# Kernel tuning notes

Hardware: AMD Instinct MI355X
Metric: run time of the kernel (lower is better)

The kernel has to match this reference:

```python
import jax, jax.numpy as jnp
import numpy as np
from jax import lax

MU = 0.1          # cfg MODEL.MU (FISTA step size)
LMBD = 0.1        # cfg MODEL.LAMBDA[0]
N_STEPS = 4       # cfg MODEL.NUM_LAYERS (unrolled FISTA iterations)
BN_EPS = 1e-5


def _norm_w(W):
    # DictBlock w_norm: each dictionary filter normalized to unit L2 norm.
    # torch does this under no_grad (in-place on .data), so the norm is a constant.
    n = jnp.sqrt(jnp.sum(W * W, axis=(1, 2, 3), keepdims=True))
    return W / lax.stop_gradient(n + 1e-12)


def _conv(x, W, stride, pad):
    return lax.conv_general_dilated(x, W, (stride, stride), [(pad, pad)] * 2,
                                    dimension_numbers=('NCHW', 'OIHW', 'NCHW'))


def _conv_t(z, W, stride, pad, out_pad):
    # torch conv_transpose2d(z, W, stride, padding=pad, output_padding=out_pad)
    k = W.shape[2]
    Wt = jnp.transpose(jnp.flip(W, (2, 3)), (1, 0, 2, 3))  # (in_ch, dict, k, k)
    p = k - 1 - pad
    return lax.conv_general_dilated(z, Wt, (1, 1), [(p, p + out_pad)] * 2,
                                    lhs_dilation=(stride, stride),
                                    dimension_numbers=('NCHW', 'OIHW', 'NCHW'))


def _shrink(c):
    # non-negative soft threshold: relu(c - lmbd*step)
    return jax.nn.relu(c - LMBD * MU)


def _dict_conv(x, W, stride):
    # Unrolled FISTA sparse coding: min_c 0.5||x - W^T c||^2 + lmbd||c||_1, c>=0
    W = _norm_w(W)
    out_pad = stride - 1
    c = _shrink(MU * _conv(x, W, stride, 1))
    c_pre = jnp.zeros_like(c)
    t = 1.0
    for _ in range(N_STEPS - 1):
        t_next = (1.0 + float(np.sqrt(1.0 + 4.0 * t * t))) / 2.0
        a = c + ((t - 1.0) / t_next) * (c - c_pre)
        c_pre = c
        r = x - _conv_t(a, W, stride, 1, out_pad)       # reconstruction residual
        c = _shrink(a + MU * _conv(r, W, stride, 1))    # proximal gradient step
        t = t_next
    return c


def _bn(x, g, b, m, v):
    # eval-mode BatchNorm2d with running stats
    scale = g * lax.rsqrt(v + BN_EPS)
    return (x - m[None, :, None, None]) * scale[None, :, None, None] + b[None, :, None, None]


def setup_inputs() -> dict:
    key = jax.random.key(0)
    ks = jax.random.split(key, 12)
    N, Cin, Cout, H = 32, 128, 256, 56
    x = jax.random.normal(ks[0], (N, Cin, H, H), jnp.float32)
    def unit_norm(W):
        return W / (jnp.sqrt(jnp.sum(W * W, axis=(1, 2, 3), keepdims=True)) + 1e-12)
    W1 = unit_norm(jax.random.normal(ks[1], (Cout, Cin, 3, 3), jnp.float32))
    W2 = unit_norm(jax.random.normal(ks[2], (Cout, Cout, 3, 3), jnp.float32))
    Wsc = jax.random.normal(ks[3], (Cout, Cin, 1, 1), jnp.float32) * 0.05
    def bn(k):
        k1, k2, k3, k4 = jax.random.split(k, 4)
        g = 1.0 + 0.1 * jax.random.normal(k1, (Cout,), jnp.float32)
        b = 0.1 * jax.random.normal(k2, (Cout,), jnp.float32)
        m = 0.1 * jax.random.normal(k3, (Cout,), jnp.float32)
        v = 0.5 + jax.random.uniform(k4, (Cout,), jnp.float32)
        return g, b, m, v
    bn1_g, bn1_b, bn1_m, bn1_v = bn(ks[4])
    bn2_g, bn2_b, bn2_m, bn2_v = bn(ks[5])
    bnsc_g, bnsc_b, bnsc_m, bnsc_v = bn(ks[6])
    return dict(x=x, W1=W1, W2=W2, Wsc=Wsc,
                bn1_g=bn1_g, bn1_b=bn1_b, bn1_m=bn1_m, bn1_v=bn1_v,
                bn2_g=bn2_g, bn2_b=bn2_b, bn2_m=bn2_m, bn2_v=bn2_v,
                bnsc_g=bnsc_g, bnsc_b=bnsc_b, bnsc_m=bnsc_m, bnsc_v=bnsc_v)


def reference(x, W1, W2, Wsc,
              bn1_g, bn1_b, bn1_m, bn1_v,
              bn2_g, bn2_b, bn2_m, bn2_v,
              bnsc_g, bnsc_b, bnsc_m, bnsc_v):
    out = _bn(_dict_conv(x, W1, 2), bn1_g, bn1_b, bn1_m, bn1_v)
    out = _bn(_dict_conv(out, W2, 1), bn2_g, bn2_b, bn2_m, bn2_v)
    sc = _bn(_conv(x, Wsc, 2, 0), bnsc_g, bnsc_b, bnsc_m, bnsc_v)
    return jax.nn.relu(out + sc)
```

## Files before the change

### kernel.cpp

```cpp
#include <hip/hip_runtime.h>
#include <math.h>

#define MU_F 0.1f
#define SHRINK_F 0.01f
#define BN_EPS_F 1e-5f

typedef _Float16 half_t;
typedef _Float16 half8 __attribute__((ext_vector_type(8)));
typedef _Float16 half4 __attribute__((ext_vector_type(4)));
typedef float f32x4 __attribute__((ext_vector_type(4)));

template<int KS, int S, int PAD, int MODE, int CAT>
__global__ __launch_bounds__(256)
void conv_reg(const half_t* __restrict__ Af, const half_t* __restrict__ Xh,
              float* __restrict__ outF, half_t* __restrict__ outH,
              const half_t* __restrict__ auxH, const half_t* __restrict__ aux3H,
              const float* __restrict__ pscale, const float* __restrict__ pbias,
              const half_t* __restrict__ zpage,
              int Cout, int Hin, int Win, int Hout, int Wout, int KT, int ptiles,
              float alpha, float beta, float delta, int relu1, int relu2)
{
    const int tid = threadIdx.x;
    const int wv = tid >> 6, ln = tid & 63;
    const int g  = blockIdx.y * 2 + (wv & 1);
    const int fr = ln & 15, rg = ln >> 4, ko8 = rg * 8;
    const int PXTOT = 25088;

    int eh = 0, ew = 0, bx = blockIdx.x;
    if (MODE == 2) { int q = bx / ptiles; bx -= q * ptiles; eh = q >> 1; ew = q & 1; }
    const int p0 = bx * 128 + (wv >> 1) * 64;

    const int Wd   = (MODE == 2) ? (Wout >> 1) : Wout;
    const int Hd   = (MODE == 2) ? (Hout >> 1) : Hout;
    const int PHWI = Hd * Wd;

    int phv[4], pwv[4], nv[4];
    unsigned vb[4];
#pragma unroll
    for (int t = 0; t < 4; ++t) {
        int px = p0 + t * 16 + fr;
        int n  = px / PHWI; int rem = px - n * PHWI;
        int ph = rem / Wd;  int pw  = rem - ph * Wd;
        nv[t] = n; phv[t] = ph; pwv[t] = pw;
        int ih0 = (MODE == 0) ? ph * S : ph;
        int iw0 = (MODE == 0) ? pw * S : pw;
        vb[t] = ((unsigned)(n * Hin + ih0) * Win + iw0) * CAT + ko8;
    }

    const half_t* Ap = Af + ((size_t)g * KT) * 2048 + ln * 8;
    f32x4 acc[4][4] = {};
    constexpr int cpt = CAT / 32;

#pragma unroll
    for (int kh = 0; kh < KS; ++kh)
#pragma unroll
    for (int kw = 0; kw < KS; ++kw) {
        int dh, dw;
        if (MODE == 0)      { dh = kh - PAD; dw = kw - PAD; }
        else if (MODE == 1) { dh = PAD - kh; dw = PAD - kw; }
        else {
            if ((((kh ^ (eh + 1)) & 1) != 0) || (((kw ^ (ew + 1)) & 1) != 0)) continue;
            dh = (eh + PAD - kh) >> 1; dw = (ew + PAD - kw) >> 1;
        }
        const int off = (dh * Win + dw) * CAT;
        const half_t* bp[4];
#pragma unroll
        for (int t = 0; t < 4; ++t) {
            int ih = ((MODE == 0) ? phv[t] * S : phv[t]) + dh;
            int iw = ((MODE == 0) ? pwv[t] * S : pwv[t]) + dw;
            bool ok = (unsigned)ih < (unsigned)Hin && (unsigned)iw < (unsigned)Win;
            bp[t] = ok ? (Xh + vb[t] + off) : zpage;
        }
        const int tap = kh * KS + kw;
        const half_t* Apt = Ap + (size_t)(tap * cpt) * 2048;
#pragma unroll
        for (int ci = 0; ci < cpt; ++ci) {
            half8 fa[4], fb[4];
#pragma unroll
            for (int m = 0; m < 4; ++m)
                fa[m] = *(const half8*)(Apt + ci * 2048 + m * 512);
#pragma unroll
            for (int t = 0; t < 4; ++t)
                fb[t] = *(const half8*)(bp[t] + ci * 32);
#pragma unroll
            for (int m = 0; m < 4; ++m)
#pragma unroll
                for (int t = 0; t < 4; ++t)
                    acc[m][t] = __builtin_amdgcn_mfma_f32_16x16x32_f16(fa[m], fb[t], acc[m][t], 0, 0, 0);
        }
    }

#pragma unroll
    for (int t = 0; t < 4; ++t) {
        int oh, ow;
        if (MODE == 2) { oh = 2 * phv[t] + eh; ow = 2 * pwv[t] + ew; }
        else           { oh = phv[t];          ow = pwv[t]; }
        size_t gb = ((size_t)(nv[t] * Hout + oh) * Wout + ow) * Cout + g * 64;
#pragma unroll
        for (int m = 0; m < 4; ++m) {
            const int cb = m * 16 + rg * 4;
            float v[4];
#pragma unroll
            for (int r = 0; r < 4; ++r) v[r] = alpha * acc[m][t][r] + delta;
            if (auxH) {
                half4 a1 = *(const half4*)(auxH + gb + cb);
#pragma unroll
                for (int r = 0; r < 4; ++r) v[r] += beta * (float)a1[r];
            }
            if (relu1)
#pragma unroll
                for (int r = 0; r < 4; ++r) v[r] = fmaxf(v[r], 0.f);
            if (pscale) {
                f32x4 s = *(const f32x4*)(pscale + g * 64 + cb);
                f32x4 b = *(const f32x4*)(pbias  + g * 64 + cb);
#pragma unroll
                for (int r = 0; r < 4; ++r) v[r] = s[r] * v[r] + b[r];
            }
            if (aux3H) {
                half4 a3 = *(const half4*)(aux3H + gb + cb);
#pragma unroll
                for (int r = 0; r < 4; ++r) v[r] += (float)a3[r];
            }
            if (relu2)
#pragma unroll
                for (int r = 0; r < 4; ++r) v[r] = fmaxf(v[r], 0.f);
            if (outH) {
                half4 o;
#pragma unroll
                for (int r = 0; r < 4; ++r) o[r] = (half_t)v[r];
                *(half4*)(outH + gb + cb) = o;
            } else {
                const int co = g * 64 + cb;
#pragma unroll
                for (int r = 0; r < 4; ++r)
                    outF[((size_t)(nv[t] * Cout + co + r) * Hout + oh) * Wout + ow] = v[r];
            }
        }
    }
}

template<int KT>
__global__ __launch_bounds__(256)
void pack_w(const float* __restrict__ W, half_t* __restrict__ Wh,
            half_t* __restrict__ WTh, int Cin, int Cout, int do_norm)
{
    __shared__ float red[256];
    int co = blockIdx.x, tid = threadIdx.x;
    int CK = Cin * KT;
    const float* w = W + (size_t)co * CK;
    float inv = 1.f;
    if (do_norm) {
        float s = 0.f;
        for (int i = tid; i < CK; i += 256) { float v = w[i]; s += v * v; }
        red[tid] = s; __syncthreads();
        for (int o = 128; o > 0; o >>= 1) {
            if (tid < o) red[tid] += red[tid + o];
            __syncthreads();
        }
        inv = 1.f / (sqrtf(red[0]) + 1e-12f);
    }
    for (int i = tid; i < CK; i += 256) {
        int ci = i / KT, tap = i - ci * KT;
        half_t h = (half_t)(w[i] * inv);
        Wh[((size_t)co * KT + tap) * Cin + ci] = h;
        if (WTh) WTh[((size_t)ci * KT + tap) * Cout + co] = h;
    }
}

__global__ __launch_bounds__(256)
void pack_frag(const half_t* __restrict__ Wflat, half_t* __restrict__ Af,
               int KT, int total8)
{
    int idx = blockIdx.x * 256 + threadIdx.x;
    if (idx >= total8) return;
    int l = idx & 63, m = (idx >> 6) & 3, t2 = idx >> 8;
    int kc = t2 % KT, gg = t2 / KT;
    int row = gg * 64 + m * 16 + (l & 15);
    int koff = kc * 32 + (l >> 4) * 8;
    int K9 = KT * 32;
    *(half8*)(Af + (size_t)idx * 8) = *(const half8*)(Wflat + (size_t)row * K9 + koff);
}

__global__ __launch_bounds__(256)
void tx_kernel(const float* __restrict__ x, half_t* __restrict__ xTh)
{
    __shared__ __align__(16) half_t tl[56 * 136];
    int h = blockIdx.x, n = blockIdx.y, tid = threadIdx.x;
    for (int it = 0; it < 28; ++it) {
        int id = tid + it * 256;
        int c = id / 56, w0 = id - c * 56;
        tl[w0 * 136 + c] = (half_t)x[(((size_t)n * 128 + c) * 56 + h) * 56 + w0];
    }
    __syncthreads();
    if (tid < 224) {
        int w0 = tid >> 2, part = tid & 3;
        size_t base = (((size_t)n * 56 + h) * 56 + w0) * 128 + part * 32;
#pragma unroll
        for (int j = 0; j < 4; ++j)
            *(half8*)(xTh + base + j * 8) = *(const half8*)(tl + w0 * 136 + part * 32 + j * 8);
    }
}

__global__ __launch_bounds__(256)
void comb_kernel(const half_t* __restrict__ c, const half_t* __restrict__ p,
                 half_t* __restrict__ a, float w1, float w2, int n8)
{
    int i = blockIdx.x * 256 + threadIdx.x;
    if (i >= n8) return;
    half8 cv = ((const half8*)c)[i];
    half8 pv = ((const half8*)p)[i];
    half8 r;
#pragma unroll
    for (int j = 0; j < 8; ++j) r[j] = (half_t)(w1 * (float)cv[j] + w2 * (float)pv[j]);
    ((half8*)a)[i] = r;
}

__global__ __launch_bounds__(256)
void bn_prep_kernel(const float* __restrict__ g, const float* __restrict__ b,
                    const float* __restrict__ m, const float* __restrict__ v,
                    float* __restrict__ s, float* __restrict__ t, int C)
{
    int i = blockIdx.x * 256 + threadIdx.x;
    if (i < C) {
        float sc = g[i] * rsqrtf(v[i] + BN_EPS_F);
        s[i] = sc; t[i] = b[i] - m[i] * sc;
    }
}

__global__ __launch_bounds__(256)
void zero_kernel(half_t* __restrict__ p, int n)
{
    int i = blockIdx.x * 256 + threadIdx.x;
    if (i < n) p[i] = (half_t)0.f;
}

extern "C" void kernel_launch(void* const* d_in, const int* in_sizes, int n_in,
                              void* d_out, int out_size, void* d_ws, size_t ws_size,
                              hipStream_t stream)
{
    (void)in_sizes; (void)n_in; (void)out_size;
    const float* x    = (const float*)d_in[0];
    const float* W1   = (const float*)d_in[1];
    const float* W2   = (const float*)d_in[2];
    const float* Wsc  = (const float*)d_in[3];
    const float* bn1g = (const float*)d_in[4];
    const float* bn1b = (const float*)d_in[5];
    const float* bn1m = (const float*)d_in[6];
    const float* bn1v = (const float*)d_in[7];
    const float* bn2g = (const float*)d_in[8];
    const float* bn2b = (const float*)d_in[9];
    const float* bn2m = (const float*)d_in[10];
    const float* bn2v = (const float*)d_in[11];
    const float* bscg = (const float*)d_in[12];
    const float* bscb = (const float*)d_in[13];
    const float* bscm = (const float*)d_in[14];
    const float* bscv = (const float*)d_in[15];

    const size_t NB = (size_t)32 * 256 * 28 * 28;
    const size_t NX = (size_t)32 * 128 * 56 * 56;

    char* base = (char*)d_ws;
    size_t off = 0;
    auto alloc = [&](size_t nbytes) -> void* {
        void* r = base + off;
        off = (off + nbytes + 255) & ~(size_t)255;
        return r;
    };
    half_t* Wh1  = (half_t*)alloc(294912 * 2);
    half_t* WTh1 = (half_t*)alloc(294912 * 2);
    half_t* Wh2  = (half_t*)alloc(589824 * 2);
    half_t* WTh2 = (half_t*)alloc(589824 * 2);
    half_t* Wsch = (half_t*)alloc(32768 * 2);
    half_t* Af1  = (half_t*)alloc(294912 * 2);
    half_t* AfT1 = (half_t*)alloc(294912 * 2);
    half_t* Af2  = (half_t*)alloc(589824 * 2);
    half_t* AfT2 = (half_t*)alloc(589824 * 2);
    half_t* Afsc = (half_t*)alloc(32768 * 2);
    float* bn1s = (float*)alloc(256 * 4);  float* bn1t = (float*)alloc(256 * 4);
    float* bn2s = (float*)alloc(256 * 4);  float* bn2t = (float*)alloc(256 * 4);
    float* bscs = (float*)alloc(256 * 4);  float* bsct = (float*)alloc(256 * 4);
    half_t* zp   = (half_t*)alloc(512 * 2);
    half_t* xTh  = (half_t*)alloc(NX * 2);
    half_t* r56h = (half_t*)alloc(NX * 2);
    half_t* Pa   = (half_t*)alloc(NB * 2);
    half_t* Pb   = (half_t*)alloc(NB * 2);
    half_t* Pc   = (half_t*)alloc(NB * 2);
    half_t* Py   = (half_t*)alloc(NB * 2);
    half_t* r28h = (half_t*)alloc(NB * 2);
    half_t* Psc  = (half_t*)alloc(NB * 2);
    if (off > ws_size) return;

    float* outp = (float*)d_out;

    double t = 1.0; float al[3];
    for (int i = 0; i < 3; ++i) {
        double tn = (1.0 + sqrt(1.0 + 4.0 * t * t)) / 2.0;
        al[i] = (float)((t - 1.0) / tn); t = tn;
    }

    const dim3 blk(256);
    const dim3 gF(196, 2);
    const dim3 gT2(784, 1);
    const int n8 = (int)(NB / 8);
    const dim3 gC((n8 + 255) / 256);
    const float* NF = nullptr;
    const half_t* NH = nullptr;
    float* NFo = nullptr;
    half_t* NHo = nullptr;

    pack_w<9><<<256, blk, 0, stream>>>(W1, Wh1, WTh1, 128, 256, 1);
    pack_w<9><<<256, blk, 0, stream>>>(W2, Wh2, WTh2, 256, 256, 1);
    pack_w<1><<<256, blk, 0, stream>>>(Wsc, Wsch, nullptr, 128, 256, 0);
    pack_frag<<<(36864 + 255) / 256, blk, 0, stream>>>(Wh1,  Af1,  36, 36864);
    pack_frag<<<(36864 + 255) / 256, blk, 0, stream>>>(WTh1, AfT1, 72, 36864);
    pack_frag<<<(73728 + 255) / 256, blk, 0, stream>>>(Wh2,  Af2,  72, 73728);
    pack_frag<<<(73728 + 255) / 256, blk, 0, stream>>>(WTh2, AfT2, 72, 73728);
    pack_frag<<<(4096  + 255) / 256, blk, 0, stream>>>(Wsch, Afsc,  4, 4096);
    bn_prep_kernel<<<1, blk, 0, stream>>>(bn1g, bn1b, bn1m, bn1v, bn1s, bn1t, 256);
    bn_prep_kernel<<<1, blk, 0, stream>>>(bn2g, bn2b, bn2m, bn2v, bn2s, bn2t, 256);
    bn_prep_kernel<<<1, blk, 0, stream>>>(bscg, bscb, bscm, bscv, bscs, bsct, 256);
    zero_kernel<<<2, blk, 0, stream>>>(zp, 512);
    tx_kernel<<<dim3(56, 32), blk, 0, stream>>>(x, xTh);

    conv_reg<3,2,1,0,128><<<gF, blk, 0, stream>>>(Af1, xTh, NFo, Pa, NH, NH, NF, NF, zp,
        256, 56, 56, 28, 28, 36, 196, MU_F, 0.f, -SHRINK_F, 1, 0);
    conv_reg<1,2,0,0,128><<<gF, blk, 0, stream>>>(Afsc, xTh, NFo, Psc, NH, NH, bscs, bsct, zp,
        256, 56, 56, 28, 28, 4, 196, 1.f, 0.f, 0.f, 0, 0);

    conv_reg<3,2,1,2,256><<<gT2, blk, 0, stream>>>(AfT1, Pa, NFo, r56h, xTh, NH, NF, NF, zp,
        128, 28, 28, 56, 56, 72, 196, -1.f, 1.f, 0.f, 0, 0);
    conv_reg<3,2,1,0,128><<<gF, blk, 0, stream>>>(Af1, r56h, NFo, Pb, Pa, NH, NF, NF, zp,
        256, 56, 56, 28, 28, 36, 196, MU_F, 1.f, -SHRINK_F, 1, 0);

    comb_kernel<<<gC, blk, 0, stream>>>(Pb, Pa, Pc, 1.f + al[1], -al[1], n8);
    conv_reg<3,2,1,2,256><<<gT2, blk, 0, stream>>>(AfT1, Pc, NFo, r56h, xTh, NH, NF, NF, zp,
        128, 28, 28, 56, 56, 72, 196, -1.f, 1.f, 0.f, 0, 0);
    conv_reg<3,2,1,0,128><<<gF, blk, 0, stream>>>(Af1, r56h, NFo, Pa, Pc, NH, NF, NF, zp,
        256, 56, 56, 28, 28, 36, 196, MU_F, 1.f, -SHRINK_F, 1, 0);

    comb_kernel<<<gC, blk, 0, stream>>>(Pa, Pb, Pc, 1.f + al[2], -al[2], n8);
    conv_reg<3,2,1,2,256><<<gT2, blk, 0, stream>>>(AfT1, Pc, NFo, r56h, xTh, NH, NF, NF, zp,
        128, 28, 28, 56, 56, 72, 196, -1.f, 1.f, 0.f, 0, 0);
    conv_reg<3,2,1,0,128><<<gF, blk, 0, stream>>>(Af1, r56h, NFo, Py, Pc, NH, bn1s, bn1t, zp,
        256, 56, 56, 28, 28, 36, 196, MU_F, 1.f, -SHRINK_F, 1, 0);

    conv_reg<3,1,1,0,256><<<gF, blk, 0, stream>>>(Af2, Py, NFo, Pa, NH, NH, NF, NF, zp,
        256, 28, 28, 28, 28, 72, 196, MU_F, 0.f, -SHRINK_F, 1, 0);

    conv_reg<3,1,1,1,256><<<gF, blk, 0, stream>>>(AfT2, Pa, NFo, r28h, Py, NH, NF, NF, zp,
        256, 28, 28, 28, 28, 72, 196, -1.f, 1.f, 0.f, 0, 0);
    conv_reg<3,1,1,0,256><<<gF, blk, 0, stream>>>(Af2, r28h, NFo, Pb, Pa, NH, NF, NF, zp,
        256, 28, 28, 28, 28, 72, 196, MU_F, 1.f, -SHRINK_F, 1, 0);

    comb_kernel<<<gC, blk, 0, stream>>>(Pb, Pa, Pc, 1.f + al[1], -al[1], n8);
    conv_reg<3,1,1,1,256><<<gF, blk, 0, stream>>>(AfT2, Pc, NFo, r28h, Py, NH, NF, NF, zp,
        256, 28, 28, 28, 28, 72, 196, -1.f, 1.f, 0.f, 0, 0);
    conv_reg<3,1,1,0,256><<<gF, blk, 0, stream>>>(Af2, r28h, NFo, Pa, Pc, NH, NF, NF, zp,
        256, 28, 28, 28, 28, 72, 196, MU_F, 1.f, -SHRINK_F, 1, 0);

    comb_kernel<<<gC, blk, 0, stream>>>(Pa, Pb, Pc, 1.f + al[2], -al[2], n8);
    conv_reg<3,1,1,1,256><<<gF, blk, 0, stream>>>(AfT2, Pc, NFo, r28h, Py, NH, NF, NF, zp,
        256, 28, 28, 28, 28, 72, 196, -1.f, 1.f, 0.f, 0, 0);
    conv_reg<3,1,1,0,256><<<gF, blk, 0, stream>>>(Af2, r28h, outp, NHo, Pc, Psc, bn2s, bn2t, zp,
        256, 28, 28, 28, 28, 72, 196, MU_F, 1.f, -SHRINK_F, 1, 1);
}
```

Measured before the change: 1.315 ms.

## Pad activations with zero halos and software-pipeline conv fragment loads

All intermediate activation buffers now carry a one-pixel zero halo, so the conv kernel drops the per-tap bounds checks and zero-page pointer selection and reads directly at padded offsets. The tap/channel loop becomes one flat loop with a four-deep register prefetch of A and B fragments, so loads for later steps are in flight while MFMAs run. Launch bounds now request one block per CU to give the extra registers room. Costs are larger buffers, extra halo-zeroing launches, and possible lower occupancy. Residual and epilogue indexing must also follow the padded layout.

```diff
diff --git a/kernel.cpp b/kernel.cpp
--- a/kernel.cpp
+++ b/kernel.cpp
@@ -11,12 +11,11 @@
 typedef float f32x4 __attribute__((ext_vector_type(4)));
 
 template<int KS, int S, int PAD, int MODE, int CAT>
-__global__ __launch_bounds__(256)
+__global__ __launch_bounds__(256, 1)
 void conv_reg(const half_t* __restrict__ Af, const half_t* __restrict__ Xh,
               float* __restrict__ outF, half_t* __restrict__ outH,
               const half_t* __restrict__ auxH, const half_t* __restrict__ aux3H,
               const float* __restrict__ pscale, const float* __restrict__ pbias,
-              const half_t* __restrict__ zpage,
               int Cout, int Hin, int Win, int Hout, int Wout, int KT, int ptiles,
               float alpha, float beta, float delta, int relu1, int relu2)
 {
@@ -24,7 +23,7 @@
     const int wv = tid >> 6, ln = tid & 63;
     const int g  = blockIdx.y * 2 + (wv & 1);
     const int fr = ln & 15, rg = ln >> 4, ko8 = rg * 8;
-    const int PXTOT = 25088;
+    const int Hp = Hin + 2, Wp = Win + 2;
 
     int eh = 0, ew = 0, bx = blockIdx.x;
     if (MODE == 2) { int q = bx / ptiles; bx -= q * ptiles; eh = q >> 1; ew = q & 1; }
@@ -34,8 +33,7 @@
     const int Hd   = (MODE == 2) ? (Hout >> 1) : Hout;
     const int PHWI = Hd * Wd;
 
-    int phv[4], pwv[4], nv[4];
-    unsigned vb[4];
+    int phv[4], pwv[4], nv[4], vb[4];
 #pragma unroll
     for (int t = 0; t < 4; ++t) {
         int px = p0 + t * 16 + fr;
@@ -44,58 +42,62 @@
         nv[t] = n; phv[t] = ph; pwv[t] = pw;
         int ih0 = (MODE == 0) ? ph * S : ph;
         int iw0 = (MODE == 0) ? pw * S : pw;
-        vb[t] = ((unsigned)(n * Hin + ih0) * Win + iw0) * CAT + ko8;
-    }
-
-    const half_t* Ap = Af + ((size_t)g * KT) * 2048 + ln * 8;
+        vb[t] = ((n * Hp + ih0 + 1) * Wp + (iw0 + 1)) * CAT + ko8;
+    }
+
+    const half_t* Ap = Af + (size_t)g * KT * 2048 + ln * 8;
+    constexpr int cpt = CAT / 32;
+    constexpr int lgc = (cpt == 8) ? 3 : 2;
+    int phh = 0, pww = 0, lgj = 0, ntap;
+    if (MODE == 2) { phh = (eh + 1) & 1; pww = (ew + 1) & 1; lgj = ew; ntap = (1 + eh) * (1 + ew); }
+    else           { ntap = KS * KS; }
+    const int total = ntap << lgc;
+
     f32x4 acc[4][4] = {};
-    constexpr int cpt = CAT / 32;
-
-#pragma unroll
-    for (int kh = 0; kh < KS; ++kh)
-#pragma unroll
-    for (int kw = 0; kw < KS; ++kw) {
+
+    auto fetch = [&](int k, half8* fa, half8* fb) {
+        const int ci = k & (cpt - 1), ti = k >> lgc;
+        int kh, kw;
+        if (MODE == 2) { int i2 = ti >> lgj, j = ti & ((1 << lgj) - 1); kh = phh + 2 * i2; kw = pww + 2 * j; }
+        else           { kh = (ti * 11) >> 5; kw = ti - 3 * kh; }
         int dh, dw;
-        if (MODE == 0)      { dh = kh - PAD; dw = kw - PAD; }
-        else if (MODE == 1) { dh = PAD - kh; dw = PAD - kw; }
-        else {
-            if ((((kh ^ (eh + 1)) & 1) != 0) || (((kw ^ (ew + 1)) & 1) != 0)) continue;
-            dh = (eh + PAD - kh) >> 1; dw = (ew + PAD - kw) >> 1;
-        }
-        const int off = (dh * Win + dw) * CAT;
-        const half_t* bp[4];
-#pragma unroll
-        for (int t = 0; t < 4; ++t) {
-            int ih = ((MODE == 0) ? phv[t] * S : phv[t]) + dh;
-            int iw = ((MODE == 0) ? pwv[t] * S : pwv[t]) + dw;
-            bool ok = (unsigned)ih < (unsigned)Hin && (unsigned)iw < (unsigned)Win;
-            bp[t] = ok ? (Xh + vb[t] + off) : zpage;
-        }
-        const int tap = kh * KS + kw;
-        const half_t* Apt = Ap + (size_t)(tap * cpt) * 2048;
-#pragma unroll
-        for (int ci = 0; ci < cpt; ++ci) {
-            half8 fa[4], fb[4];
-#pragma unroll
-            for (int m = 0; m < 4; ++m)
-                fa[m] = *(const half8*)(Apt + ci * 2048 + m * 512);
+        if (MODE == 0)      { dh = kh - PAD;        dw = kw - PAD; }
+        else if (MODE == 1) { dh = PAD - kh;        dw = PAD - kw; }
+        else                { dh = (eh + PAD - kh) >> 1; dw = (ew + PAD - kw) >> 1; }
+        const int off = (dh * Wp + dw) * CAT + (ci << 5);
+#pragma unroll
+        for (int t = 0; t < 4; ++t)
+            fb[t] = *(const half8*)(Xh + (vb[t] + off));
+        const int akc = (MODE == 2) ? ((kh * KS + kw) * cpt + ci) : k;
+        const half_t* Apk = Ap + (size_t)akc * 2048;
+#pragma unroll
+        for (int m = 0; m < 4; ++m)
+            fa[m] = *(const half8*)(Apk + m * 512);
+    };
+    auto mfma16 = [&](half8* fa, half8* fb) {
+#pragma unroll
+        for (int m = 0; m < 4; ++m)
 #pragma unroll
             for (int t = 0; t < 4; ++t)
-                fb[t] = *(const half8*)(bp[t] + ci * 32);
-#pragma unroll
-            for (int m = 0; m < 4; ++m)
-#pragma unroll
-                for (int t = 0; t < 4; ++t)
-                    acc[m][t] = __builtin_amdgcn_mfma_f32_16x16x32_f16(fa[m], fb[t], acc[m][t], 0, 0, 0);
-        }
-    }
-
+                acc[m][t] = __builtin_amdgcn_mfma_f32_16x16x32_f16(fa[m], fb[t], acc[m][t], 0, 0, 0);
+    };
+
+    half8 A0[4], B0[4], A1[4], B1[4], A2[4], B2[4], A3[4], B3[4];
+    fetch(0, A0, B0); fetch(1, A1, B1); fetch(2, A2, B2); fetch(3, A3, B3);
+    for (int k = 0; k < total; k += 4) {
+        mfma16(A0, B0); if (k + 4 < total) fetch(k + 4, A0, B0);
+        mfma16(A1, B1); if (k + 5 < total) fetch(k + 5, A1, B1);
+        mfma16(A2, B2); if (k + 6 < total) fetch(k + 6, A2, B2);
+        mfma16(A3, B3); if (k + 7 < total) fetch(k + 7, A3, B3);
+    }
+
+    const int Hpo = Hout + 2, Wpo = Wout + 2;
 #pragma unroll
     for (int t = 0; t < 4; ++t) {
         int oh, ow;
         if (MODE == 2) { oh = 2 * phv[t] + eh; ow = 2 * pwv[t] + ew; }
         else           { oh = phv[t];          ow = pwv[t]; }
-        size_t gb = ((size_t)(nv[t] * Hout + oh) * Wout + ow) * Cout + g * 64;
+        size_t gb = ((size_t)(nv[t] * Hpo + oh + 1) * Wpo + (ow + 1)) * Cout + g * 64;
 #pragma unroll
         for (int m = 0; m < 4; ++m) {
             const int cb = m * 16 + rg * 4;
@@ -194,10 +196,27 @@
     __syncthreads();
     if (tid < 224) {
         int w0 = tid >> 2, part = tid & 3;
-        size_t base = (((size_t)n * 56 + h) * 56 + w0) * 128 + part * 32;
+        size_t base = (((size_t)n * 58 + h + 1) * 58 + (w0 + 1)) * 128 + part * 32;
 #pragma unroll
         for (int j = 0; j < 4; ++j)
             *(half8*)(xTh + base + j * 8) = *(const half8*)(tl + w0 * 136 + part * 32 + j * 8);
+    }
+}
+
+__global__ __launch_bounds__(256)
+void halo_zero(half_t* __restrict__ p, int Hp, int Wp, int C)
+{
+    int n = blockIdx.y;
+    size_t base = (size_t)n * Hp * Wp * C;
+    int per = 2 * Wp + 2 * (Hp - 2);
+    int tot = per * C;
+    for (int i = blockIdx.x * 256 + threadIdx.x; i < tot; i += gridDim.x * 256) {
+        int pos = i / C, c = i - pos * C;
+        int h, w;
+        if (pos < Wp)            { h = 0;      w = pos; }
+        else if (pos < 2 * Wp)   { h = Hp - 1; w = pos - Wp; }
+        else { int r = pos - 2 * Wp; h = 1 + (r >> 1); w = (r & 1) ? (Wp - 1) : 0; }
+        p[base + ((size_t)h * Wp + w) * C + c] = (half_t)0.f;
     }
 }
 
@@ -225,13 +244,6 @@
         float sc = g[i] * rsqrtf(v[i] + BN_EPS_F);
         s[i] = sc; t[i] = b[i] - m[i] * sc;
     }
-}
-
-__global__ __launch_bounds__(256)
-void zero_kernel(half_t* __restrict__ p, int n)
-{
-    int i = blockIdx.x * 256 + threadIdx.x;
-    if (i < n) p[i] = (half_t)0.f;
 }
 
 extern "C" void kernel_launch(void* const* d_in, const int* in_sizes, int n_in,
@@ -256,8 +268,8 @@
     const float* bscm = (const float*)d_in[14];
     const float* bscv = (const float*)d_in[15];
 
-    const size_t NB = (size_t)32 * 256 * 28 * 28;
-    const size_t NX = (size_t)32 * 128 * 56 * 56;
+    const size_t P56 = (size_t)32 * 58 * 58 * 128;
+    const size_t P28 = (size_t)32 * 30 * 30 * 256;
 
     char* base = (char*)d_ws;
     size_t off = 0;
@@ -279,15 +291,14 @@
     float* bn1s = (float*)alloc(256 * 4);  float* bn1t = (float*)alloc(256 * 4);
     float* bn2s = (float*)alloc(256 * 4);  float* bn2t = (float*)alloc(256 * 4);
     float* bscs = (float*)alloc(256 * 4);  float* bsct = (float*)alloc(256 * 4);
-    half_t* zp   = (half_t*)alloc(512 * 2);
-    half_t* xTh  = (half_t*)alloc(NX * 2);
-    half_t* r56h = (half_t*)alloc(NX * 2);
-    half_t* Pa   = (half_t*)alloc(NB * 2);
-    half_t* Pb   = (half_t*)alloc(NB * 2);
-    half_t* Pc   = (half_t*)alloc(NB * 2);
-    half_t* Py   = (half_t*)alloc(NB * 2);
-    half_t* r28h = (half_t*)alloc(NB * 2);
-    half_t* Psc  = (half_t*)alloc(NB * 2);
+    half_t* xTh  = (half_t*)alloc(P56 * 2);
+    half_t* r56h = (half_t*)alloc(P56 * 2);
+    half_t* Pa   = (half_t*)alloc(P28 * 2);
+    half_t* Pb   = (half_t*)alloc(P28 * 2);
+    half_t* Pc   = (half_t*)alloc(P28 * 2);
+    half_t* Py   = (half_t*)alloc(P28 * 2);
+    half_t* r28h = (half_t*)alloc(P28 * 2);
+    half_t* Psc  = (half_t*)alloc(P28 * 2);
     if (off > ws_size) return;
 
     float* outp = (float*)d_out;
@@ -301,7 +312,7 @@
     const dim3 blk(256);
     const dim3 gF(196, 2);
     const dim3 gT2(784, 1);
-    const int n8 = (int)(NB / 8);
+    const int n8 = (int)(P28 / 8);
     const dim3 gC((n8 + 255) / 256);
     const float* NF = nullptr;
     const half_t* NH = nullptr;
@@ -319,48 +330,54 @@
     bn_prep_kernel<<<1, blk, 0, stream>>>(bn1g, bn1b, bn1m, bn1v, bn1s, bn1t, 256);
     bn_prep_kernel<<<1, blk, 0, stream>>>(bn2g, bn2b, bn2m, bn2v, bn2s, bn2t, 256);
     bn_prep_kernel<<<1, blk, 0, stream>>>(bscg, bscb, bscm, bscv, bscs, bsct, 256);
-    zero_kernel<<<2, blk, 0, stream>>>(zp, 512);
+    halo_zero<<<dim3(8, 32), blk, 0, stream>>>(xTh,  58, 58, 128);
+    halo_zero<<<dim3(8, 32), blk, 0, stream>>>(r56h, 58, 58, 128);
+    halo_zero<<<dim3(8, 32), blk, 0, stream>>>(Pa,   30, 30, 256);
+    halo_zero<<<dim3(8, 32), blk, 0, stream>>>(Pb,   30, 30, 256);
+    halo_zero<<<dim3(8, 32), blk, 0, stream>>>(Pc,   30, 30, 256);
+    halo_zero<<<dim3(8, 32), blk, 0, stream>>>(Py,   30, 30, 256);
+    halo_zero<<<dim3(8, 32), blk, 0, stream>>>(r28h, 30, 30, 256);
     tx_kernel<<<dim3(56, 32), blk, 0, stream>>>(x, xTh);
 
-    conv_reg<3,2,1,0,128><<<gF, blk, 0, stream>>>(Af1, xTh, NFo, Pa, NH, NH, NF, NF, zp,
+    conv_reg<3,2,1,0,128><<<gF, blk, 0, stream>>>(Af1, xTh, NFo, Pa, NH, NH, NF, NF,
         256, 56, 56, 28, 28, 36, 196, MU_F, 0.f, -SHRINK_F, 1, 0);
-    conv_reg<1,2,0,0,128><<<gF, blk, 0, stream>>>(Afsc, xTh, NFo, Psc, NH, NH, bscs, bsct, zp,
+    conv_reg<1,2,0,0,128><<<gF, blk, 0, stream>>>(Afsc, xTh, NFo, Psc, NH, NH, bscs, bsct,
         256, 56, 56, 28, 28, 4, 196, 1.f, 0.f, 0.f, 0, 0);
 
-    conv_reg<3,2,1,2,256><<<gT2, blk, 0, stream>>>(AfT1, Pa, NFo, r56h, xTh, NH, NF, NF, zp,
+    conv_reg<3,2,1,2,256><<<gT2, blk, 0, stream>>>(AfT1, Pa, NFo, r56h, xTh, NH, NF, NF,
         128, 28, 28, 56, 56, 72, 196, -1.f, 1.f, 0.f, 0, 0);
-    conv_reg<3,2,1,0,128><<<gF, blk, 0, stream>>>(Af1, r56h, NFo, Pb, Pa, NH, NF, NF, zp,
+    conv_reg<3,2,1,0,128><<<gF, blk, 0, stream>>>(Af1, r56h, NFo, Pb, Pa, NH, NF, NF,
         256, 56, 56, 28, 28, 36, 196, MU_F, 1.f, -SHRINK_F, 1, 0);
 
     comb_kernel<<<gC, blk, 0, stream>>>(Pb, Pa, Pc, 1.f + al[1], -al[1], n8);
-    conv_reg<3,2,1,2,256><<<gT2, blk, 0, stream>>>(AfT1, Pc, NFo, r56h, xTh, NH, NF, NF, zp,
+    conv_reg<3,2,1,2,256><<<gT2, blk, 0, stream>>>(AfT1, Pc, NFo, r56h, xTh, NH, NF, NF,
         128, 28, 28, 56, 56, 72, 196, -1.f, 1.f, 0.f, 0, 0);
-    conv_reg<3,2,1,0,128><<<gF, blk, 0, stream>>>(Af1, r56h, NFo, Pa, Pc, NH, NF, NF, zp,
+    conv_reg<3,2,1,0,128><<<gF, blk, 0, stream>>>(Af1, r56h, NFo, Pa, Pc, NH, NF, NF,
         256, 56, 56, 28, 28, 36, 196, MU_F, 1.f, -SHRINK_F, 1, 0);
 
     comb_kernel<<<gC, blk, 0, stream>>>(Pa, Pb, Pc, 1.f + al[2], -al[2], n8);
-    conv_reg<3,2,1,2,256><<<gT2, blk, 0, stream>>>(AfT1, Pc, NFo, r56h, xTh, NH, NF, NF, zp,
+    conv_reg<3,2,1,2,256><<<gT2, blk, 0, stream>>>(AfT1, Pc, NFo, r56h, xTh, NH, NF, NF,
         128, 28, 28, 56, 56, 72, 196, -1.f, 1.f, 0.f, 0, 0);
-    conv_reg<3,2,1,0,128><<<gF, blk, 0, stream>>>(Af1, r56h, NFo, Py, Pc, NH, bn1s, bn1t, zp,
+    conv_reg<3,2,1,0,128><<<gF, blk, 0, stream>>>(Af1, r56h, NFo, Py, Pc, NH, bn1s, bn1t,
         256, 56, 56, 28, 28, 36, 196, MU_F, 1.f, -SHRINK_F, 1, 0);
 
-    conv_reg<3,1,1,0,256><<<gF, blk, 0, stream>>>(Af2, Py, NFo, Pa, NH, NH, NF, NF, zp,
+    conv_reg<3,1,1,0,256><<<gF, blk, 0, stream>>>(Af2, Py, NFo, Pa, NH, NH, NF, NF,
         256, 28, 28, 28, 28, 72, 196, MU_F, 0.f, -SHRINK_F, 1, 0);
 
-    conv_reg<3,1,1,1,256><<<gF, blk, 0, stream>>>(AfT2, Pa, NFo, r28h, Py, NH, NF, NF, zp,
+    conv_reg<3,1,1,1,256><<<gF, blk, 0, stream>>>(AfT2, Pa, NFo, r28h, Py, NH, NF, NF,
         256, 28, 28, 28, 28, 72, 196, -1.f, 1.f, 0.f, 0, 0);
-    conv_reg<3,1,1,0,256><<<gF, blk, 0, stream>>>(Af2, r28h, NFo, Pb, Pa, NH, NF, NF, zp,
+    conv_reg<3,1,1,0,256><<<gF, blk, 0, stream>>>(Af2, r28h, NFo, Pb, Pa, NH, NF, NF,
         256, 28, 28, 28, 28, 72, 196, MU_F, 1.f, -SHRINK_F, 1, 0);
 
     comb_kernel<<<gC, blk, 0, stream>>>(Pb, Pa, Pc, 1.f + al[1], -al[1], n8);
-    conv_reg<3,1,1,1,256><<<gF, blk, 0, stream>>>(AfT2, Pc, NFo, r28h, Py, NH, NF, NF, zp,
+    conv_reg<3,1,1,1,256><<<gF, blk, 0, stream>>>(AfT2, Pc, NFo, r28h, Py, NH, NF, NF,
         256, 28, 28, 28, 28, 72, 196, -1.f, 1.f, 0.f, 0, 0);
-    conv_reg<3,1,1,0,256><<<gF, blk, 0, stream>>>(Af2, r28h, NFo, Pa, Pc, NH, NF, NF, zp,
+    conv_reg<3,1,1,0,256><<<gF, blk, 0, stream>>>(Af2, r28h, NFo, Pa, Pc, NH, NF, NF,
         256, 28, 28, 28, 28, 72, 196, MU_F, 1.f, -SHRINK_F, 1, 0);
 
     comb_kernel<<<gC, blk, 0, stream>>>(Pa, Pb, Pc, 1.f + al[2], -al[2], n8);
-    conv_reg<3,1,1,1,256><<<gF, blk, 0, stream>>>(AfT2, Pc, NFo, r28h, Py, NH, NF, NF, zp,
+    conv_reg<3,1,1,1,256><<<gF, blk, 0, stream>>>(AfT2, Pc, NFo, r28h, Py, NH, NF, NF,
         256, 28, 28, 28, 28, 72, 196, -1.f, 1.f, 0.f, 0, 0);
-    conv_reg<3,1,1,0,256><<<gF, blk, 0, stream>>>(Af2, r28h, outp, NHo, Pc, Psc, bn2s, bn2t, zp,
+    conv_reg<3,1,1,0,256><<<gF, blk, 0, stream>>>(Af2, r28h, outp, NHo, Pc, Psc, bn2s, bn2t,
         256, 28, 28, 28, 28, 72, 196, MU_F, 1.f, -SHRINK_F, 1, 1);
 }
```

New measurement: 1.337 ms. About the same (+1.7%).
